# Performance work log

Hardware: AMD Instinct MI355X
Metric: run time of the kernel (lower is better)

## Reference

```python
import jax, jax.numpy as jnp
import numpy as np

EPS = 1e-5
NHEAD = 8
TOP_K = 2


def _layernorm(x, g, b):
    m = jnp.mean(x, axis=-1, keepdims=True)
    v = jnp.mean((x - m) ** 2, axis=-1, keepdims=True)
    return (x - m) * jax.lax.rsqrt(v + EPS) * g + b


def setup_inputs() -> dict:
    S, D, F, E = 4096, 512, 2048, 8
    key = jax.random.key(0)
    ks = jax.random.split(key, 18)
    std = 0.02
    return {
        "src": jax.random.normal(ks[0], (S, D), jnp.float32),
        "in_proj_w": std * jax.random.normal(ks[1], (3 * D, D), jnp.float32),
        "in_proj_b": jnp.zeros((3 * D,), jnp.float32),
        "out_proj_w": std * jax.random.normal(ks[2], (D, D), jnp.float32),
        "out_proj_b": jnp.zeros((D,), jnp.float32),
        "ln1_g": jnp.ones((D,), jnp.float32),
        "ln1_b": jnp.zeros((D,), jnp.float32),
        "ln2_g": jnp.ones((D,), jnp.float32),
        "ln2_b": jnp.zeros((D,), jnp.float32),
        "gate_w": std * jax.random.normal(ks[3], (E, D), jnp.float32),
        "gate_b": jnp.zeros((E,), jnp.float32),
        "w1": std * jax.random.normal(ks[4], (E, F, D), jnp.float32),
        "b1": jnp.zeros((E, F), jnp.float32),
        "w2": std * jax.random.normal(ks[5], (E, F, D), jnp.float32),
        "b2": jnp.zeros((E, F), jnp.float32),
        "wo": std * jax.random.normal(ks[6], (E, D, F), jnp.float32),
        "bo": jnp.zeros((E, D), jnp.float32),
    }


def _sa_block(x, in_proj_w, in_proj_b, out_proj_w, out_proj_b):
    # x: [S, D] unbatched sequence (torch MultiheadAttention unbatched path)
    S, D = x.shape
    hd = D // NHEAD
    qkv = x @ in_proj_w.T + in_proj_b              # [S, 3D]
    q, k, v = jnp.split(qkv, 3, axis=-1)
    q = q.reshape(S, NHEAD, hd)
    k = k.reshape(S, NHEAD, hd)
    v = v.reshape(S, NHEAD, hd)
    scores = jnp.einsum("shd,thd->hst", q, k) / jnp.sqrt(jnp.float32(hd))
    attn = jax.nn.softmax(scores, axis=-1)         # [H, S, S]
    out = jnp.einsum("hst,thd->shd", attn, v).reshape(S, D)
    return out @ out_proj_w.T + out_proj_b


def _ff_block(x, gate_w, gate_b, w1, b1, w2, b2, wo, bo):
    # top-k gated SwiGLU MoE; gate probs are softmax, NOT renormalized after topk
    T = x.shape[0]
    E = w1.shape[0]
    gates = jax.nn.softmax(x @ gate_w.T + gate_b, axis=-1)      # [T, E]
    top_scores, top_idx = jax.lax.top_k(gates, TOP_K)            # [T, k]
    combine = jnp.zeros((T, E), x.dtype).at[
        jnp.arange(T)[:, None], top_idx].add(top_scores)         # [T, E]
    out = jnp.zeros_like(x)
    for e in range(E):  # small fixed expert count
        h = jax.nn.silu(x @ w1[e].T + b1[e]) * (x @ w2[e].T + b2[e])
        out = out + combine[:, e:e + 1] * (h @ wo[e].T + bo[e])
    return out


def reference(src, in_proj_w, in_proj_b, out_proj_w, out_proj_b,
              ln1_g, ln1_b, ln2_g, ln2_b,
              gate_w, gate_b, w1, b1, w2, b2, wo, bo):
    # norm_first pre-norm residual layer, dropout=0 (eval)
    x = src
    x = x + _sa_block(_layernorm(x, ln1_g, ln1_b),
                      in_proj_w, in_proj_b, out_proj_w, out_proj_b)
    x = x + _ff_block(_layernorm(x, ln2_g, ln2_b),
                      gate_w, gate_b, w1, b1, w2, b2, wo, bo)
    return x
```

## Files before the change

kernel.cpp:

```cpp
#include <hip/hip_runtime.h>
#include <hip/hip_bf16.h>
#include <math.h>

#define SQ   4096
#define DM   512
#define NH   8
#define HDIM 64
#define FF   2048
#define NE   8

typedef unsigned short u16;
typedef unsigned int   u32;
typedef __attribute__((ext_vector_type(8))) __bf16 bf16x8;
typedef __attribute__((ext_vector_type(4))) float  f32x4;

__device__ __forceinline__ float bf2f(u16 v) {
    union { u32 i; float f; } c; c.i = ((u32)v) << 16; return c.f;
}
__device__ __forceinline__ u16 f2bf(float f) {
    union { float f; u32 i; } c; c.f = f; u32 u = c.i;
    return (u16)((u + 0x7fffu + ((u >> 16) & 1u)) >> 16);
}

#define BM 128
#define BN 128
#define BK 32
#define BKP 40

__global__ __launch_bounds__(256) void gemm_split(
    const u16* __restrict__ Ahi, const u16* __restrict__ Alo, int lda,
    const u16* __restrict__ Bhi, const u16* __restrict__ Blo, int ldb,
    int M, int N, int K,
    const float* __restrict__ bias,
    const float* __restrict__ resid, int ldres,
    u16* __restrict__ Chi, u16* __restrict__ Clo,
    float* __restrict__ Cf, int ldc, int mode)
{
    __shared__ __align__(16) u16 Ash[BM * BKP], Asl[BM * BKP];
    __shared__ __align__(16) u16 Bsh[BN * BKP], Bsl[BN * BKP];
    const int tid  = threadIdx.x;
    const int wave = tid >> 6;
    const int lane = tid & 63;
    const int quad = lane >> 4;
    const int l16  = lane & 15;
    const int bm = blockIdx.x * BM;
    const int bn = blockIdx.y * BN;
    const int wm = (wave & 1) * 64;
    const int wn = (wave >> 1) * 64;

    f32x4 acc[4][4];
#pragma unroll
    for (int i = 0; i < 4; i++)
#pragma unroll
        for (int j = 0; j < 4; j++)
#pragma unroll
            for (int r = 0; r < 4; r++) acc[i][j][r] = 0.0f;

    for (int k0 = 0; k0 < K; k0 += BK) {
#pragma unroll
        for (int i = 0; i < 2; i++) {
            int c = tid + i * 256;
            int row = c >> 2;
            int col = (c & 3) << 3;
            int ga = bm + row, gb2 = bn + row;
            uint4 vah = make_uint4(0u,0u,0u,0u), val = vah, vbh = vah, vbl = vah;
            if (ga < M) {
                vah = *(const uint4*)(Ahi + (size_t)ga * lda + k0 + col);
                val = *(const uint4*)(Alo + (size_t)ga * lda + k0 + col);
            }
            if (gb2 < N) {
                vbh = *(const uint4*)(Bhi + (size_t)gb2 * ldb + k0 + col);
                vbl = *(const uint4*)(Blo + (size_t)gb2 * ldb + k0 + col);
            }
            *(uint4*)(Ash + row * BKP + col) = vah;
            *(uint4*)(Asl + row * BKP + col) = val;
            *(uint4*)(Bsh + row * BKP + col) = vbh;
            *(uint4*)(Bsl + row * BKP + col) = vbl;
        }
        __syncthreads();
        bf16x8 ah[4], al[4], bh[4], bl[4];
#pragma unroll
        for (int i = 0; i < 4; i++) {
            ah[i] = *(const bf16x8*)(Ash + (wm + i * 16 + l16) * BKP + quad * 8);
            al[i] = *(const bf16x8*)(Asl + (wm + i * 16 + l16) * BKP + quad * 8);
        }
#pragma unroll
        for (int j = 0; j < 4; j++) {
            bh[j] = *(const bf16x8*)(Bsh + (wn + j * 16 + l16) * BKP + quad * 8);
            bl[j] = *(const bf16x8*)(Bsl + (wn + j * 16 + l16) * BKP + quad * 8);
        }
#pragma unroll
        for (int i = 0; i < 4; i++)
#pragma unroll
            for (int j = 0; j < 4; j++) {
                acc[i][j] = __builtin_amdgcn_mfma_f32_16x16x32_bf16(ah[i], bh[j], acc[i][j], 0,0,0);
                acc[i][j] = __builtin_amdgcn_mfma_f32_16x16x32_bf16(ah[i], bl[j], acc[i][j], 0,0,0);
                acc[i][j] = __builtin_amdgcn_mfma_f32_16x16x32_bf16(al[i], bh[j], acc[i][j], 0,0,0);
            }
        __syncthreads();
    }

#pragma unroll
    for (int i = 0; i < 4; i++)
#pragma unroll
        for (int j = 0; j < 4; j++)
#pragma unroll
            for (int r = 0; r < 4; r++) {
                int row = bm + wm + i * 16 + quad * 4 + r;
                int col = bn + wn + j * 16 + l16;
                if (row >= M || col >= N) continue;
                float v = acc[i][j][r] + (bias ? bias[col] : 0.0f);
                size_t idx = (size_t)row * ldc + col;
                if (mode == 0) {
                    u16 hb = f2bf(v);
                    Chi[idx] = hb;
                    Clo[idx] = f2bf(v - bf2f(hb));
                } else {
                    if (resid) v += resid[(size_t)row * ldres + col];
                    Cf[idx] = v;
                }
            }
}

__global__ __launch_bounds__(256) void moe12_all(
    const u16* __restrict__ A, int lda,
    const int* __restrict__ idxl, const int* __restrict__ cnt,
    const int* __restrict__ off,
    const float* __restrict__ w1, const float* __restrict__ b1,
    const float* __restrict__ w2, const float* __restrict__ b2,
    u16* __restrict__ H)
{
    const int bmg = blockIdx.x * BM;
    if (bmg >= off[NE]) return;
    int e = 0;
    while (e < NE - 1 && bmg >= off[e + 1]) e++;
    const int M   = cnt[e];
    const int bml = bmg - off[e];
    if (bml >= M) return;
    const float* B1 = w1 + (size_t)e * FF * DM;
    const float* B2 = w2 + (size_t)e * FF * DM;
    const int*   rl = idxl + e * SQ;

    __shared__ __align__(16) u16 As[BM * BKP], Bs1[BN * BKP], Bs2[BN * BKP];
    const int tid  = threadIdx.x;
    const int wave = tid >> 6;
    const int lane = tid & 63;
    const int quad = lane >> 4;
    const int l16  = lane & 15;
    const int bn = blockIdx.y * BN;
    const int wm = (wave & 1) * 64;
    const int wn = (wave >> 1) * 64;

    f32x4 acc1[4][4], acc2[4][4];
#pragma unroll
    for (int i = 0; i < 4; i++)
#pragma unroll
        for (int j = 0; j < 4; j++)
#pragma unroll
            for (int r = 0; r < 4; r++) { acc1[i][j][r] = 0.0f; acc2[i][j][r] = 0.0f; }

    for (int k0 = 0; k0 < DM; k0 += BK) {
#pragma unroll
        for (int i = 0; i < 2; i++) {
            int c = tid + i * 256;
            int row = c >> 2;
            int col = (c & 3) << 3;
            uint4 va = make_uint4(0u,0u,0u,0u);
            int lr = bml + row;
            if (lr < M) {
                int ar = rl[lr];
                va = *(const uint4*)(A + (size_t)ar * lda + k0 + col);
            }
            *(uint4*)(As + row * BKP + col) = va;
        }
#pragma unroll
        for (int i = 0; i < 4; i++) {
            int c = tid + i * 256;
            int row = c >> 3;
            int col = (c & 7) << 2;
            float4 v1 = *(const float4*)(B1 + (size_t)(bn + row) * DM + k0 + col);
            float4 v2 = *(const float4*)(B2 + (size_t)(bn + row) * DM + k0 + col);
            ushort4 h1, h2;
            h1.x = f2bf(v1.x); h1.y = f2bf(v1.y); h1.z = f2bf(v1.z); h1.w = f2bf(v1.w);
            h2.x = f2bf(v2.x); h2.y = f2bf(v2.y); h2.z = f2bf(v2.z); h2.w = f2bf(v2.w);
            *(ushort4*)(Bs1 + row * BKP + col) = h1;
            *(ushort4*)(Bs2 + row * BKP + col) = h2;
        }
        __syncthreads();
        bf16x8 af[4], b1f[4], b2f[4];
#pragma unroll
        for (int i = 0; i < 4; i++)
            af[i] = *(const bf16x8*)(As + (wm + i * 16 + l16) * BKP + quad * 8);
#pragma unroll
        for (int j = 0; j < 4; j++) {
            b1f[j] = *(const bf16x8*)(Bs1 + (wn + j * 16 + l16) * BKP + quad * 8);
            b2f[j] = *(const bf16x8*)(Bs2 + (wn + j * 16 + l16) * BKP + quad * 8);
        }
#pragma unroll
        for (int i = 0; i < 4; i++)
#pragma unroll
            for (int j = 0; j < 4; j++) {
                acc1[i][j] = __builtin_amdgcn_mfma_f32_16x16x32_bf16(af[i], b1f[j], acc1[i][j], 0,0,0);
                acc2[i][j] = __builtin_amdgcn_mfma_f32_16x16x32_bf16(af[i], b2f[j], acc2[i][j], 0,0,0);
            }
        __syncthreads();
    }

#pragma unroll
    for (int i = 0; i < 4; i++)
#pragma unroll
        for (int j = 0; j < 4; j++)
#pragma unroll
            for (int r = 0; r < 4; r++) {
                int rowl = bml + wm + i * 16 + quad * 4 + r;
                if (rowl >= M) continue;
                int col = bn + wn + j * 16 + l16;
                float g1 = acc1[i][j][r] + b1[e * FF + col];
                float g2 = acc2[i][j][r] + b2[e * FF + col];
                float s  = g1 / (1.0f + __expf(-g1));
                H[(size_t)(off[e] + rowl) * FF + col] = f2bf(s * g2);
            }
}

__global__ __launch_bounds__(256) void moe_y_all(
    const u16* __restrict__ H,
    const float* __restrict__ wo, const float* __restrict__ bo,
    const int* __restrict__ idxl, const float* __restrict__ cw,
    const int* __restrict__ cnt, const int* __restrict__ off,
    float* __restrict__ out)
{
    const int bmg = blockIdx.x * BM;
    if (bmg >= off[NE]) return;
    int e = 0;
    while (e < NE - 1 && bmg >= off[e + 1]) e++;
    const int M   = cnt[e];
    const int bml = bmg - off[e];
    if (bml >= M) return;
    const float* B = wo + (size_t)e * DM * FF;

    __shared__ __align__(16) u16 As[BM * BKP], Bs[BN * BKP];
    const int tid  = threadIdx.x;
    const int wave = tid >> 6;
    const int lane = tid & 63;
    const int quad = lane >> 4;
    const int l16  = lane & 15;
    const int bn = blockIdx.y * BN;
    const int wm = (wave & 1) * 64;
    const int wn = (wave >> 1) * 64;

    f32x4 acc[4][4];
#pragma unroll
    for (int i = 0; i < 4; i++)
#pragma unroll
        for (int j = 0; j < 4; j++)
#pragma unroll
            for (int r = 0; r < 4; r++) acc[i][j][r] = 0.0f;

    for (int k0 = 0; k0 < FF; k0 += BK) {
#pragma unroll
        for (int i = 0; i < 2; i++) {
            int c = tid + i * 256;
            int row = c >> 2;
            int col = (c & 3) << 3;
            uint4 va = *(const uint4*)(H + (size_t)(bmg + row) * FF + k0 + col);
            *(uint4*)(As + row * BKP + col) = va;
        }
#pragma unroll
        for (int i = 0; i < 4; i++) {
            int c = tid + i * 256;
            int row = c >> 3;
            int col = (c & 7) << 2;
            float4 v = *(const float4*)(B + (size_t)(bn + row) * FF + k0 + col);
            ushort4 h;
            h.x = f2bf(v.x); h.y = f2bf(v.y); h.z = f2bf(v.z); h.w = f2bf(v.w);
            *(ushort4*)(Bs + row * BKP + col) = h;
        }
        __syncthreads();
        bf16x8 af[4], bf[4];
#pragma unroll
        for (int i = 0; i < 4; i++)
            af[i] = *(const bf16x8*)(As + (wm + i * 16 + l16) * BKP + quad * 8);
#pragma unroll
        for (int j = 0; j < 4; j++)
            bf[j] = *(const bf16x8*)(Bs + (wn + j * 16 + l16) * BKP + quad * 8);
#pragma unroll
        for (int i = 0; i < 4; i++)
#pragma unroll
            for (int j = 0; j < 4; j++)
                acc[i][j] = __builtin_amdgcn_mfma_f32_16x16x32_bf16(af[i], bf[j], acc[i][j], 0,0,0);
        __syncthreads();
    }

#pragma unroll
    for (int i = 0; i < 4; i++)
#pragma unroll
        for (int j = 0; j < 4; j++)
#pragma unroll
            for (int r = 0; r < 4; r++) {
                int rowl = bml + wm + i * 16 + quad * 4 + r;
                if (rowl >= M) continue;
                int col = bn + wn + j * 16 + l16;
                int tok = idxl[e * SQ + rowl];
                float wgt = cw[e * SQ + rowl];
                atomicAdd(out + (size_t)tok * DM + col,
                          wgt * (acc[i][j][r] + bo[e * DM + col]));
            }
}

#define KP 72
#define SCL 0.18033688011112042f

template <int SPLIT>
__device__ __forceinline__ void flash_body(
    const u16* __restrict__ qh, const u16* __restrict__ ql,
    const u16* __restrict__ vth, const u16* __restrict__ vtl,
    u16* __restrict__ oh, u16* __restrict__ ol,
    float* __restrict__ Opart, float* __restrict__ mpart,
    float* __restrict__ lpart)
{
    __shared__ __align__(16) u16 Ksh[64*KP], Ksl[64*KP], Vsh[64*KP], Vsl[64*KP];
    const int tid  = threadIdx.x;
    const int wave = tid >> 6;
    const int lane = tid & 63;
    const int quad = lane >> 4;
    const int l16  = lane & 15;
    const int h    = blockIdx.y;
    const int z    = (SPLIT > 1) ? blockIdx.z : 0;
    const int qbase = blockIdx.x * 64 + wave * 16;

    u16* const Pwh = Ksh + wave * (16 * KP);
    u16* const Pwl = Ksl + wave * (16 * KP);

    bf16x8 aqh[2], aql[2];
#pragma unroll
    for (int kk = 0; kk < 2; kk++) {
        size_t off = (size_t)(qbase + l16) * (3*DM) + h*HDIM + kk*32 + quad*8;
        aqh[kk] = *(const bf16x8*)(qh + off);
        aql[kk] = *(const bf16x8*)(ql + off);
    }

    float m_[4], l_[4];
    f32x4 o_[4];
#pragma unroll
    for (int r = 0; r < 4; r++) { m_[r] = -1e30f; l_[r] = 0.0f; }
#pragma unroll
    for (int nd = 0; nd < 4; nd++)
#pragma unroll
        for (int r = 0; r < 4; r++) o_[nd][r] = 0.0f;

    const int NT = SQ / 64 / SPLIT;
    for (int jt = z * NT; jt < (z + 1) * NT; jt++) {
#pragma unroll
        for (int i = 0; i < 2; i++) {
            int c = tid + i * 256;
            int r = c >> 3;
            int co = (c & 7) << 3;
            size_t koff = (size_t)(jt*64 + r) * (3*DM) + DM + h*HDIM + co;
            size_t voff = (size_t)(h*HDIM + r) * SQ + jt*64 + co;
            *(uint4*)(Ksh + r*KP + co) = *(const uint4*)(qh + koff);
            *(uint4*)(Ksl + r*KP + co) = *(const uint4*)(ql + koff);
            *(uint4*)(Vsh + r*KP + co) = *(const uint4*)(vth + voff);
            *(uint4*)(Vsl + r*KP + co) = *(const uint4*)(vtl + voff);
        }
        __syncthreads();

        f32x4 s[4];
#pragma unroll
        for (int jn = 0; jn < 4; jn++) {
            f32x4 zz;
#pragma unroll
            for (int r = 0; r < 4; r++) zz[r] = 0.0f;
#pragma unroll
            for (int kk = 0; kk < 2; kk++) {
                bf16x8 kh = *(const bf16x8*)(Ksh + (jn*16 + l16)*KP + kk*32 + quad*8);
                bf16x8 kl = *(const bf16x8*)(Ksl + (jn*16 + l16)*KP + kk*32 + quad*8);
                zz = __builtin_amdgcn_mfma_f32_16x16x32_bf16(aqh[kk], kh, zz, 0,0,0);
                zz = __builtin_amdgcn_mfma_f32_16x16x32_bf16(aqh[kk], kl, zz, 0,0,0);
                zz = __builtin_amdgcn_mfma_f32_16x16x32_bf16(aql[kk], kh, zz, 0,0,0);
            }
#pragma unroll
            for (int r = 0; r < 4; r++) zz[r] *= SCL;
            s[jn] = zz;
        }
        __syncthreads();

        float mx[4], al2[4], rs[4];
#pragma unroll
        for (int r = 0; r < 4; r++)
            mx[r] = fmaxf(fmaxf(s[0][r], s[1][r]), fmaxf(s[2][r], s[3][r]));
#pragma unroll
        for (int r = 0; r < 4; r++) {
#pragma unroll
            for (int o2 = 1; o2 < 16; o2 <<= 1)
                mx[r] = fmaxf(mx[r], __shfl_xor(mx[r], o2));
            float nm = fmaxf(m_[r], mx[r]);
            al2[r] = exp2f(m_[r] - nm);
            m_[r] = nm;
            rs[r] = 0.0f;
        }
#pragma unroll
        for (int jn = 0; jn < 4; jn++)
#pragma unroll
            for (int r = 0; r < 4; r++) {
                float p = exp2f(s[jn][r] - m_[r]);
                s[jn][r] = p;
                rs[r] += p;
            }
#pragma unroll
        for (int r = 0; r < 4; r++) {
#pragma unroll
            for (int o2 = 1; o2 < 16; o2 <<= 1)
                rs[r] += __shfl_xor(rs[r], o2);
            l_[r] = l_[r] * al2[r] + rs[r];
        }
#pragma unroll
        for (int nd = 0; nd < 4; nd++)
#pragma unroll
            for (int r = 0; r < 4; r++) o_[nd][r] *= al2[r];
#pragma unroll
        for (int jn = 0; jn < 4; jn++)
#pragma unroll
            for (int r = 0; r < 4; r++) {
                float p = s[jn][r];
                u16 ph = f2bf(p);
                int pidx = (quad*4 + r)*KP + jn*16 + l16;
                Pwh[pidx] = ph;
                Pwl[pidx] = f2bf(p - bf2f(ph));
            }

        bf16x8 ph[2], pl[2];
#pragma unroll
        for (int kk = 0; kk < 2; kk++) {
            ph[kk] = *(const bf16x8*)(Pwh + l16*KP + kk*32 + quad*8);
            pl[kk] = *(const bf16x8*)(Pwl + l16*KP + kk*32 + quad*8);
        }
#pragma unroll
        for (int nd = 0; nd < 4; nd++) {
#pragma unroll
            for (int kk = 0; kk < 2; kk++) {
                bf16x8 vh = *(const bf16x8*)(Vsh + (nd*16 + l16)*KP + kk*32 + quad*8);
                bf16x8 vl = *(const bf16x8*)(Vsl + (nd*16 + l16)*KP + kk*32 + quad*8);
                o_[nd] = __builtin_amdgcn_mfma_f32_16x16x32_bf16(ph[kk], vh, o_[nd], 0,0,0);
                o_[nd] = __builtin_amdgcn_mfma_f32_16x16x32_bf16(ph[kk], vl, o_[nd], 0,0,0);
                o_[nd] = __builtin_amdgcn_mfma_f32_16x16x32_bf16(pl[kk], vh, o_[nd], 0,0,0);
            }
        }
        __syncthreads();
    }

    if (SPLIT == 1) {
#pragma unroll
        for (int nd = 0; nd < 4; nd++)
#pragma unroll
            for (int r = 0; r < 4; r++) {
                int row = qbase + quad*4 + r;
                int col = h*HDIM + nd*16 + l16;
                float w = o_[nd][r] / l_[r];
                u16 hb = f2bf(w);
                oh[(size_t)row * DM + col] = hb;
                ol[(size_t)row * DM + col] = f2bf(w - bf2f(hb));
            }
    } else {
#pragma unroll
        for (int nd = 0; nd < 4; nd++)
#pragma unroll
            for (int r = 0; r < 4; r++) {
                int row = qbase + quad*4 + r;
                int col = h*HDIM + nd*16 + l16;
                Opart[((size_t)z * SQ + row) * DM + col] = o_[nd][r];
            }
        if (l16 == 0) {
#pragma unroll
            for (int r = 0; r < 4; r++) {
                int row = qbase + quad*4 + r;
                mpart[(z*NH + h) * SQ + row] = m_[r];
                lpart[(z*NH + h) * SQ + row] = l_[r];
            }
        }
    }
}

__global__ __launch_bounds__(256) void flash_attn(
    const u16* __restrict__ qh, const u16* __restrict__ ql,
    const u16* __restrict__ vth, const u16* __restrict__ vtl,
    u16* __restrict__ oh, u16* __restrict__ ol)
{
    flash_body<1>(qh, ql, vth, vtl, oh, ol, nullptr, nullptr, nullptr);
}

__global__ __launch_bounds__(256) void flash_attn_part(
    const u16* __restrict__ qh, const u16* __restrict__ ql,
    const u16* __restrict__ vth, const u16* __restrict__ vtl,
    float* __restrict__ Opart, float* __restrict__ mpart,
    float* __restrict__ lpart)
{
    flash_body<2>(qh, ql, vth, vtl, nullptr, nullptr, Opart, mpart, lpart);
}

__global__ __launch_bounds__(256) void attn_combine(
    const float* __restrict__ Opart, const float* __restrict__ mpart,
    const float* __restrict__ lpart,
    u16* __restrict__ oh, u16* __restrict__ ol)
{
    const int row = blockIdx.x;
    const int tid = threadIdx.x;
#pragma unroll
    for (int i = 0; i < 2; i++) {
        int col = tid + i * 256;
        int h = col >> 6;
        float m0 = mpart[h * SQ + row];
        float m1 = mpart[(NH + h) * SQ + row];
        float l0 = lpart[h * SQ + row];
        float l1 = lpart[(NH + h) * SQ + row];
        float m  = fmaxf(m0, m1);
        float a0 = exp2f(m0 - m);
        float a1 = exp2f(m1 - m);
        float O  = Opart[(size_t)row * DM + col] * a0
                 + Opart[((size_t)SQ + row) * DM + col] * a1;
        float l  = l0 * a0 + l1 * a1;
        float w  = O / l;
        u16 hb = f2bf(w);
        oh[(size_t)row * DM + col] = hb;
        ol[(size_t)row * DM + col] = f2bf(w - bf2f(hb));
    }
}

__global__ __launch_bounds__(256) void ln1_split(
    const float* __restrict__ x, const float* __restrict__ g,
    const float* __restrict__ b, u16* __restrict__ ohi, u16* __restrict__ olo)
{
    const int row = blockIdx.x;
    const int tid = threadIdx.x;
    float v0 = x[(size_t)row * DM + tid];
    float v1 = x[(size_t)row * DM + tid + 256];
    float s = v0 + v1, sq = v0*v0 + v1*v1;
#pragma unroll
    for (int o = 1; o < 64; o <<= 1) { s += __shfl_xor(s, o); sq += __shfl_xor(sq, o); }
    __shared__ float ss[4], ssq[4];
    if ((tid & 63) == 0) { ss[tid>>6] = s; ssq[tid>>6] = sq; }
    __syncthreads();
    s  = ss[0]+ss[1]+ss[2]+ss[3];
    sq = ssq[0]+ssq[1]+ssq[2]+ssq[3];
    float m = s * (1.0f/DM);
    float rstd = rsqrtf(sq*(1.0f/DM) - m*m + 1e-5f);
    float y0 = (v0-m)*rstd*g[tid]     + b[tid];
    float y1 = (v1-m)*rstd*g[tid+256] + b[tid+256];
    u16 h0 = f2bf(y0), h1 = f2bf(y1);
    ohi[(size_t)row*DM + tid]       = h0;  olo[(size_t)row*DM + tid]       = f2bf(y0 - bf2f(h0));
    ohi[(size_t)row*DM + tid + 256] = h1;  olo[(size_t)row*DM + tid + 256] = f2bf(y1 - bf2f(h1));
}

__global__ __launch_bounds__(256) void ln_kernel(
    const float* __restrict__ x, const float* __restrict__ g,
    const float* __restrict__ b, u16* __restrict__ out)
{
    const int row = blockIdx.x;
    const int tid = threadIdx.x;
    float v0 = x[(size_t)row * DM + tid];
    float v1 = x[(size_t)row * DM + tid + 256];
    float s = v0 + v1, sq = v0*v0 + v1*v1;
#pragma unroll
    for (int o = 1; o < 64; o <<= 1) { s += __shfl_xor(s, o); sq += __shfl_xor(sq, o); }
    __shared__ float ss[4], ssq[4];
    if ((tid & 63) == 0) { ss[tid>>6] = s; ssq[tid>>6] = sq; }
    __syncthreads();
    s  = ss[0]+ss[1]+ss[2]+ss[3];
    sq = ssq[0]+ssq[1]+ssq[2]+ssq[3];
    float m = s * (1.0f/DM);
    float rstd = rsqrtf(sq*(1.0f/DM) - m*m + 1e-5f);
    out[(size_t)row*DM + tid]       = f2bf((v0-m)*rstd*g[tid]     + b[tid]);
    out[(size_t)row*DM + tid + 256] = f2bf((v1-m)*rstd*g[tid+256] + b[tid+256]);
}

__global__ __launch_bounds__(256) void transpose_v2(
    const u16* __restrict__ qh, const u16* __restrict__ ql,
    u16* __restrict__ vth, u16* __restrict__ vtl)
{
    __shared__ u16 Th[64 * 66], Tl[64 * 66];
    const int t0  = blockIdx.x * 64;
    const int hd0 = blockIdx.y * 64;
    const int tid = threadIdx.x;
#pragma unroll
    for (int k = 0; k < 16; k++) {
        int idx = tid + k * 256;
        int r = idx >> 6, j = idx & 63;
        size_t src = (size_t)(t0 + r) * (3*DM) + 2*DM + hd0 + j;
        Th[r * 66 + j] = qh[src];
        Tl[r * 66 + j] = ql[src];
    }
    __syncthreads();
#pragma unroll
    for (int k = 0; k < 16; k++) {
        int idx = tid + k * 256;
        int r = idx >> 6, c2 = idx & 63;
        size_t dst = (size_t)(hd0 + r) * SQ + t0 + c2;
        vth[dst] = Th[c2 * 66 + r];
        vtl[dst] = Tl[c2 * 66 + r];
    }
}

__global__ __launch_bounds__(256) void gate_route(
    const float* __restrict__ x1, const float* __restrict__ g,
    const float* __restrict__ b, const float* __restrict__ gw,
    const float* __restrict__ gb,
    int* __restrict__ cnt, int* __restrict__ idxl, float* __restrict__ cw)
{
    const int token = blockIdx.x * 4 + (threadIdx.x >> 6);
    const int lane  = threadIdx.x & 63;
    const float* xr = x1 + (size_t)token * DM;
    float v[8];
#pragma unroll
    for (int i = 0; i < 8; i++) v[i] = xr[lane*8 + i];
    float s = 0.f, sq = 0.f;
#pragma unroll
    for (int i = 0; i < 8; i++) { s += v[i]; sq += v[i]*v[i]; }
#pragma unroll
    for (int o = 1; o < 64; o <<= 1) { s += __shfl_xor(s, o); sq += __shfl_xor(sq, o); }
    float m = s * (1.0f/DM);
    float rstd = rsqrtf(sq*(1.0f/DM) - m*m + 1e-5f);
    float xn[8];
#pragma unroll
    for (int i = 0; i < 8; i++)
        xn[i] = (v[i]-m)*rstd*g[lane*8+i] + b[lane*8+i];
    float logit[8];
#pragma unroll
    for (int e = 0; e < 8; e++) {
        float t = 0.f;
#pragma unroll
        for (int i = 0; i < 8; i++) t += xn[i] * gw[e*DM + lane*8 + i];
#pragma unroll
        for (int o = 1; o < 64; o <<= 1) t += __shfl_xor(t, o);
        logit[e] = t + gb[e];
    }
    if (lane == 0) {
        float mx = -1e30f;
        for (int e = 0; e < 8; e++) mx = fmaxf(mx, logit[e]);
        float den = 0.f, p[8];
        for (int e = 0; e < 8; e++) { p[e] = __expf(logit[e] - mx); den += p[e]; }
        for (int e = 0; e < 8; e++) p[e] /= den;
        int i1 = 0;
        for (int e = 1; e < 8; e++) if (p[e] > p[i1]) i1 = e;
        int i2 = -1;
        for (int e = 0; e < 8; e++) { if (e == i1) continue; if (i2 < 0 || p[e] > p[i2]) i2 = e; }
        int s1 = atomicAdd(&cnt[i1], 1);
        idxl[i1*SQ + s1] = token;  cw[i1*SQ + s1] = p[i1];
        int s2 = atomicAdd(&cnt[i2], 1);
        idxl[i2*SQ + s2] = token;  cw[i2*SQ + s2] = p[i2];
    }
}

__global__ __launch_bounds__(256) void cvt_split_w(
    const float* __restrict__ w, u16* __restrict__ wh, u16* __restrict__ wl, int n)
{
    int i = blockIdx.x * 256 + threadIdx.x;
    if (i < n) {
        float v = w[i];
        u16 h = f2bf(v);
        wh[i] = h;
        wl[i] = f2bf(v - bf2f(h));
    }
}

__global__ __launch_bounds__(64) void zero_cnt(int* cnt)
{
    if (threadIdx.x < NE) cnt[threadIdx.x] = 0;
}

__global__ __launch_bounds__(64) void make_off(const int* __restrict__ cnt,
                                              int* __restrict__ off)
{
    if (threadIdx.x == 0) {
        int a = 0;
        for (int e = 0; e < NE; e++) {
            off[e] = a;
            a += ((cnt[e] + 127) >> 7) << 7;
        }
        off[NE] = a;
    }
}

__global__ __launch_bounds__(256) void init_out(
    const float* __restrict__ x1, float* __restrict__ out)
{
    int i = blockIdx.x * 256 + threadIdx.x;
    ((float4*)out)[i] = ((const float4*)x1)[i];
}

__global__ __launch_bounds__(256) void sentinel_kernel(float* out, float v, int n)
{
    int i = blockIdx.x * 256 + threadIdx.x;
    if (i < n) out[i] = v;
}
__global__ __launch_bounds__(256) void scrub_kernel(float* out, int n)
{
    int i = blockIdx.x * 256 + threadIdx.x;
    if (i < n) { float v = out[i]; if (!isfinite(v)) out[i] = 777.0f; }
}

extern "C" void kernel_launch(void* const* d_in, const int* in_sizes, int n_in,
                              void* d_out, int out_size, void* d_ws, size_t ws_size,
                              hipStream_t stream)
{
    const float* src        = (const float*)d_in[0];
    const float* in_proj_w  = (const float*)d_in[1];
    const float* in_proj_b  = (const float*)d_in[2];
    const float* out_proj_w = (const float*)d_in[3];
    const float* out_proj_b = (const float*)d_in[4];
    const float* ln1_g      = (const float*)d_in[5];
    const float* ln1_b      = (const float*)d_in[6];
    const float* ln2_g      = (const float*)d_in[7];
    const float* ln2_b      = (const float*)d_in[8];
    const float* gate_w     = (const float*)d_in[9];
    const float* gate_b     = (const float*)d_in[10];
    const float* w1         = (const float*)d_in[11];
    const float* b1         = (const float*)d_in[12];
    const float* w2         = (const float*)d_in[13];
    const float* b2         = (const float*)d_in[14];
    const float* wo         = (const float*)d_in[15];
    const float* bo         = (const float*)d_in[16];
    float* out = (float*)d_out;

    const size_t MB = (size_t)1 << 20;
    const size_t ROUTE = 512 * 1024;
    const size_t NEED     = ROUTE + 44 * MB;
    const size_t NEED_BIG = ROUTE + 61 * MB;
    if (ws_size < NEED) {
        sentinel_kernel<<<(SQ*DM)/256, 256, 0, stream>>>(out, 333.0f, SQ*DM);
        return;
    }
    const bool big = (ws_size >= NEED_BIG);

    char* ws = (char*)d_ws;
    int*   cnt  = (int*)ws;
    int*   offp = (int*)(ws + 64);
    int*   idxl = (int*)(ws + 1024);
    float* cw   = (float*)(ws + 1024 + 128*1024);
    char*  base = ws + ROUTE;
    u16* xln1h = (u16*)(base);
    u16* xln1l = (u16*)(base + 4*MB);
    u16* attnh = (u16*)(base);
    u16* attnl = (u16*)(base + 4*MB);
    u16* qkvh  = (u16*)(base + 8*MB);
    u16* qkvl  = (u16*)(base + 20*MB);
    float* x1  = (float*)(base + 8*MB);
    u16* vth   = (u16*)(base + 32*MB);
    u16* vtl   = (u16*)(base + 36*MB);
    u16* xln2  = (u16*)(base + 36*MB);
    u16* Hbuf  = (u16*)(base);
    u16* wph   = (u16*)(base + 40*MB);
    u16* wpl   = (u16*)(base + 40*MB + 1536*1024);
    u16* woh   = (u16*)(base + 43*MB);
    u16* wol   = (u16*)(base + 43*MB + 512*1024);
    float* Opart = (float*)(base + 44*MB);
    float* mpart = (float*)(base + 60*MB);
    float* lpart = (float*)(base + 60*MB + 256*1024);

    cvt_split_w<<<(3*DM*DM)/256, 256, 0, stream>>>(in_proj_w,  wph, wpl, 3*DM*DM);
    cvt_split_w<<<(DM*DM)/256,   256, 0, stream>>>(out_proj_w, woh, wol, DM*DM);

    ln1_split<<<SQ, 256, 0, stream>>>(src, ln1_g, ln1_b, xln1h, xln1l);
    gemm_split<<<dim3(32, 12), 256, 0, stream>>>(
        xln1h, xln1l, DM, wph, wpl, DM, SQ, 3*DM, DM,
        in_proj_b, nullptr, 0, qkvh, qkvl, nullptr, 3*DM, 0);
    transpose_v2<<<dim3(SQ/64, DM/64), 256, 0, stream>>>(qkvh, qkvl, vth, vtl);
    if (big) {
        flash_attn_part<<<dim3(SQ/64, NH, 2), 256, 0, stream>>>(
            qkvh, qkvl, vth, vtl, Opart, mpart, lpart);
        attn_combine<<<SQ, 256, 0, stream>>>(Opart, mpart, lpart, attnh, attnl);
    } else {
        flash_attn<<<dim3(SQ/64, NH), 256, 0, stream>>>(
            qkvh, qkvl, vth, vtl, attnh, attnl);
    }
    gemm_split<<<dim3(32, 4), 256, 0, stream>>>(
        attnh, attnl, DM, woh, wol, DM, SQ, DM, DM,
        out_proj_b, src, DM, nullptr, nullptr, x1, DM, 1);

    ln_kernel<<<SQ, 256, 0, stream>>>(x1, ln2_g, ln2_b, xln2);
    zero_cnt<<<1, 64, 0, stream>>>(cnt);
    gate_route<<<SQ/4, 256, 0, stream>>>(x1, ln2_g, ln2_b, gate_w, gate_b,
                                         cnt, idxl, cw);
    make_off<<<1, 64, 0, stream>>>(cnt, offp);
    init_out<<<(SQ*DM/4)/256, 256, 0, stream>>>(x1, out);
    moe12_all<<<dim3(72, 16), 256, 0, stream>>>(
        xln2, DM, idxl, cnt, offp, w1, b1, w2, b2, Hbuf);
    moe_y_all<<<dim3(72, 4), 256, 0, stream>>>(
        Hbuf, wo, bo, idxl, cw, cnt, offp, out);

    scrub_kernel<<<(SQ*DM)/256, 256, 0, stream>>>(out, SQ*DM);
}
```

Measured before the change: 819.8 us.

## Prefetch next K/V tile into registers, lazy softmax rescale, and MFMA priority hints

Flash attention now loads the next K/V tile into registers while the current tile is computed, which hides global memory latency behind the MFMA work. The online-softmax rescale of O and l is skipped unless some row's max grows by more than 8 in log2 units, saving exp and multiply work per tile. s_setprio hints are placed around the MFMA sections, f2bf switches to the native __bf16 conversion, and the attention kernels get a 4-blocks-per-CU launch-bounds occupancy hint. The register prefetch raises register pressure, which may conflict with the occupancy hint. Without rescaling, p values can reach up to 2^8, which remains numerically safe in fp32 accumulation.

```diff
diff --git a/kernel.cpp b/kernel.cpp
--- a/kernel.cpp
+++ b/kernel.cpp
@@ -18,8 +18,7 @@
     union { u32 i; float f; } c; c.i = ((u32)v) << 16; return c.f;
 }
 __device__ __forceinline__ u16 f2bf(float f) {
-    union { float f; u32 i; } c; c.f = f; u32 u = c.i;
-    return (u16)((u + 0x7fffu + ((u >> 16) & 1u)) >> 16);
+    union { __bf16 h; u16 u; } c; c.h = (__bf16)f; return c.u;
 }
 
 #define BM 128
@@ -331,6 +330,9 @@
     u16* const Pwh = Ksh + wave * (16 * KP);
     u16* const Pwl = Ksl + wave * (16 * KP);
 
+    const int r_st  = tid >> 3;
+    const int co_st = (tid & 7) << 3;
+
     bf16x8 aqh[2], aql[2];
 #pragma unroll
     for (int kk = 0; kk < 2; kk++) {
@@ -348,23 +350,42 @@
 #pragma unroll
         for (int r = 0; r < 4; r++) o_[nd][r] = 0.0f;
 
-    const int NT = SQ / 64 / SPLIT;
-    for (int jt = z * NT; jt < (z + 1) * NT; jt++) {
-#pragma unroll
-        for (int i = 0; i < 2; i++) {
-            int c = tid + i * 256;
-            int r = c >> 3;
-            int co = (c & 7) << 3;
-            size_t koff = (size_t)(jt*64 + r) * (3*DM) + DM + h*HDIM + co;
-            size_t voff = (size_t)(h*HDIM + r) * SQ + jt*64 + co;
-            *(uint4*)(Ksh + r*KP + co) = *(const uint4*)(qh + koff);
-            *(uint4*)(Ksl + r*KP + co) = *(const uint4*)(ql + koff);
-            *(uint4*)(Vsh + r*KP + co) = *(const uint4*)(vth + voff);
-            *(uint4*)(Vsl + r*KP + co) = *(const uint4*)(vtl + voff);
-        }
+    const int NT    = SQ / 64 / SPLIT;
+    const int jtBeg = z * NT, jtEnd = (z + 1) * NT;
+
+    uint4 ga0, ga1, ga2, ga3, gb0, gb1, gb2, gb3;
+    auto load_tile = [&](int jt) {
+        size_t koff0 = (size_t)(jt*64 + r_st) * (3*DM) + DM + h*HDIM + co_st;
+        size_t voff0 = (size_t)(h*HDIM + r_st) * SQ + jt*64 + co_st;
+        ga0 = *(const uint4*)(qh  + koff0);
+        ga1 = *(const uint4*)(ql  + koff0);
+        ga2 = *(const uint4*)(vth + voff0);
+        ga3 = *(const uint4*)(vtl + voff0);
+        size_t koff1 = koff0 + (size_t)32 * (3*DM);
+        size_t voff1 = voff0 + (size_t)32 * SQ;
+        gb0 = *(const uint4*)(qh  + koff1);
+        gb1 = *(const uint4*)(ql  + koff1);
+        gb2 = *(const uint4*)(vth + voff1);
+        gb3 = *(const uint4*)(vtl + voff1);
+    };
+
+    load_tile(jtBeg);
+
+    for (int jt = jtBeg; jt < jtEnd; jt++) {
+        *(uint4*)(Ksh + r_st*KP + co_st)      = ga0;
+        *(uint4*)(Ksl + r_st*KP + co_st)      = ga1;
+        *(uint4*)(Vsh + r_st*KP + co_st)      = ga2;
+        *(uint4*)(Vsl + r_st*KP + co_st)      = ga3;
+        *(uint4*)(Ksh + (r_st+32)*KP + co_st) = gb0;
+        *(uint4*)(Ksl + (r_st+32)*KP + co_st) = gb1;
+        *(uint4*)(Vsh + (r_st+32)*KP + co_st) = gb2;
+        *(uint4*)(Vsl + (r_st+32)*KP + co_st) = gb3;
         __syncthreads();
 
+        if (jt + 1 < jtEnd) load_tile(jt + 1);
+
         f32x4 s[4];
+        __builtin_amdgcn_s_setprio(1);
 #pragma unroll
         for (int jn = 0; jn < 4; jn++) {
             f32x4 zz;
@@ -382,22 +403,33 @@
             for (int r = 0; r < 4; r++) zz[r] *= SCL;
             s[jn] = zz;
         }
+        __builtin_amdgcn_s_setprio(0);
         __syncthreads();
 
-        float mx[4], al2[4], rs[4];
-#pragma unroll
-        for (int r = 0; r < 4; r++)
+        float mx[4];
+#pragma unroll
+        for (int r = 0; r < 4; r++) {
             mx[r] = fmaxf(fmaxf(s[0][r], s[1][r]), fmaxf(s[2][r], s[3][r]));
-#pragma unroll
-        for (int r = 0; r < 4; r++) {
 #pragma unroll
             for (int o2 = 1; o2 < 16; o2 <<= 1)
                 mx[r] = fmaxf(mx[r], __shfl_xor(mx[r], o2));
-            float nm = fmaxf(m_[r], mx[r]);
-            al2[r] = exp2f(m_[r] - nm);
-            m_[r] = nm;
-            rs[r] = 0.0f;
-        }
+        }
+        int grew = (mx[0] > m_[0] + 8.0f) | (mx[1] > m_[1] + 8.0f) |
+                   (mx[2] > m_[2] + 8.0f) | (mx[3] > m_[3] + 8.0f);
+        if (__any(grew)) {
+#pragma unroll
+            for (int r = 0; r < 4; r++) {
+                float nm  = fmaxf(m_[r], mx[r]);
+                float al2 = exp2f(m_[r] - nm);
+                m_[r] = nm;
+                l_[r] *= al2;
+#pragma unroll
+                for (int nd = 0; nd < 4; nd++) o_[nd][r] *= al2;
+            }
+        }
+        float rs[4];
+#pragma unroll
+        for (int r = 0; r < 4; r++) rs[r] = 0.0f;
 #pragma unroll
         for (int jn = 0; jn < 4; jn++)
 #pragma unroll
@@ -411,12 +443,8 @@
 #pragma unroll
             for (int o2 = 1; o2 < 16; o2 <<= 1)
                 rs[r] += __shfl_xor(rs[r], o2);
-            l_[r] = l_[r] * al2[r] + rs[r];
-        }
-#pragma unroll
-        for (int nd = 0; nd < 4; nd++)
-#pragma unroll
-            for (int r = 0; r < 4; r++) o_[nd][r] *= al2[r];
+            l_[r] += rs[r];
+        }
 #pragma unroll
         for (int jn = 0; jn < 4; jn++)
 #pragma unroll
@@ -434,6 +462,7 @@
             ph[kk] = *(const bf16x8*)(Pwh + l16*KP + kk*32 + quad*8);
             pl[kk] = *(const bf16x8*)(Pwl + l16*KP + kk*32 + quad*8);
         }
+        __builtin_amdgcn_s_setprio(1);
 #pragma unroll
         for (int nd = 0; nd < 4; nd++) {
 #pragma unroll
@@ -445,6 +474,7 @@
                 o_[nd] = __builtin_amdgcn_mfma_f32_16x16x32_bf16(pl[kk], vh, o_[nd], 0,0,0);
             }
         }
+        __builtin_amdgcn_s_setprio(0);
         __syncthreads();
     }
 
@@ -480,7 +510,7 @@
     }
 }
 
-__global__ __launch_bounds__(256) void flash_attn(
+__global__ __launch_bounds__(256, 4) void flash_attn(
     const u16* __restrict__ qh, const u16* __restrict__ ql,
     const u16* __restrict__ vth, const u16* __restrict__ vtl,
     u16* __restrict__ oh, u16* __restrict__ ol)
@@ -488,7 +518,7 @@
     flash_body<1>(qh, ql, vth, vtl, oh, ol, nullptr, nullptr, nullptr);
 }
 
-__global__ __launch_bounds__(256) void flash_attn_part(
+__global__ __launch_bounds__(256, 4) void flash_attn_part(
     const u16* __restrict__ qh, const u16* __restrict__ ql,
     const u16* __restrict__ vth, const u16* __restrict__ vtl,
     float* __restrict__ Opart, float* __restrict__ mpart,
```

Result: faster. 801.2 us (-2.3%).
